# Performance work log

Measured on AMD Instinct MI355X. Metric: run time of the kernel, lower is better.

Reference implementation:

```python
import jax, jax.numpy as jnp
import numpy as np

D, T, HID, Q = 33, 49, 64, 64


def _lin(x, w, b):
    return x @ w.T + b


def setup_inputs() -> dict:
    key = jax.random.key(0)
    ks = jax.random.split(key, 40)

    def nrm(k, shape, scale=0.1):
        return jax.random.normal(k, shape, jnp.float32) * scale

    vals = nrm(ks[0], (D, T), 1.0)
    mask = (jax.random.uniform(ks[1], (D, T)) < 0.8).astype(jnp.float32)
    delta = jax.random.uniform(ks[2], (D, T)) * 2.0
    data = jnp.stack([vals, mask, delta])  # [3, 33, 49]

    return {
        "data": data,
        "h0": nrm(ks[3], (HID,), 1.0),
        "H0": nrm(ks[4], (D, HID), 1.0),
        "gh_w": nrm(ks[5], (HID, D)), "gh_b": nrm(ks[6], (HID,)),
        "gst_w": nrm(ks[7], (HID, D)), "gst_b": nrm(ks[8], (HID,)),
        "gru_wih": nrm(ks[9], (3 * HID, D)), "gru_whh": nrm(ks[10], (3 * HID, HID)),
        "gru_bih": nrm(ks[11], (3 * HID,)), "gru_bhh": nrm(ks[12], (3 * HID,)),
        "wu0_w": nrm(ks[13], (Q, HID)), "wu0_b": nrm(ks[14], (Q,)),
        "wu1_w": nrm(ks[15], (Q, 2 * HID)), "wu1_b": nrm(ks[16], (Q,)),
        "wu_w": nrm(ks[17], (Q, 3 * HID)), "wu_b": nrm(ks[18], (Q,)),
        "wh_w": nrm(ks[19], (D, HID + Q)), "wh_b": nrm(ks[20], (D,)),
        "xst_w": nrm(ks[21], (1, HID)), "xst_b": nrm(ks[22], (1,)),
        "wrg_w": nrm(ks[23], (D, HID)),
        "wrs": nrm(ks[24], (1, HID)),
        "tWz": nrm(ks[25], (D, HID, HID)), "tUzx": nrm(ks[26], (D, HID, 1)), "tUzh": nrm(ks[27], (D, HID, HID)),
        "tWr": nrm(ks[28], (D, HID, HID)), "tUrx": nrm(ks[29], (D, HID, 1)), "tUrh": nrm(ks[30], (D, HID, HID)),
        "tWh": nrm(ks[31], (D, HID, HID)), "tUhx": nrm(ks[32], (D, HID, 1)), "tUhh": nrm(ks[33], (D, HID, HID)),
        "tbz": nrm(ks[34], (HID, 1)), "tbr": nrm(ks[35], (HID, 1)), "tbh": nrm(ks[36], (HID, 1)),
    }


def reference(data, h0, H0, gh_w, gh_b, gst_w, gst_b, gru_wih, gru_whh,
              gru_bih, gru_bhh, wu0_w, wu0_b, wu1_w, wu1_b, wu_w, wu_b,
              wh_w, wh_b, xst_w, xst_b, wrg_w, wrs, tWz, tUzx, tUzh,
              tWr, tUrx, tUrh, tWh, tUhx, tUhh, tbz, tbr, tbh):
    X, M, Dt = data[0], data[1], data[2]  # each (33, 49)
    h = h0          # (HID,) -> becomes (1, HID) after first GRUCell step
    H = H0          # (D, HID)
    outs, Hs, xps = [], [], []
    for t in range(T):
        x, m, d = X[:, t], M[:, t], Dt[:, t]
        # GRU-D style decay gate: exp(-max(0, Linear(delta)))
        gamma_h = jnp.exp(-jax.nn.relu(_lin(d, gh_w, gh_b)))
        h = gamma_h * h
        x_st = _lin(H, xst_w, xst_b).reshape(-1)       # (D,)
        x_st_c = m * x + (1 - m) * x_st                # imputed input
        # torch nn.GRUCell
        xi = x_st_c.reshape(1, D)
        hi = h.reshape(1, HID)
        gi = _lin(xi, gru_wih, gru_bih)
        gh_ = _lin(hi, gru_whh, gru_bhh)
        i_r, i_z, i_n = jnp.split(gi, 3, axis=1)
        h_r, h_z, h_n = jnp.split(gh_, 3, axis=1)
        r = jax.nn.sigmoid(i_r + h_r)
        z = jax.nn.sigmoid(i_z + h_z)
        n = jnp.tanh(i_n + r * h_n)
        h = (1 - z) * n + z * hi                       # (1, HID)
        # original detaches the history used for u_t
        outs.append(jax.lax.stop_gradient(h))
        if t == 0:
            u_t = _lin(h0.reshape(1, -1), wu0_w, wu0_b)
        elif t == 1:
            hd = jnp.concatenate([h0.reshape(1, -1), outs[0]], 0).reshape(1, -1)
            u_t = _lin(hd, wu1_w, wu1_b)
        elif t == 2:
            hd = jnp.concatenate([h0.reshape(1, -1), outs[0], outs[1]], 0).reshape(1, -1)
            u_t = _lin(hd, wu_w, wu_b)
        else:
            hd = jnp.concatenate(outs[t - 3:t], 0).reshape(1, -1)
            u_t = _lin(hd, wu_w, wu_b)
        x_gt_hat = _lin(jnp.concatenate([h, u_t], axis=1), wh_w, wh_b)  # (1, D)
        gamma_st = jnp.exp(-jax.nn.relu(_lin(d, gst_w, gst_b)))
        H = gamma_st * H
        # tMGRU cell: per-variable (D=33) batched matmuls
        Hr = H[:, :, None]              # (D, HID, 1)
        xr = x_st_c[:, None, None]      # (D, 1, 1)
        hr = h.reshape(HID, 1)          # (HID, 1)
        z_t = jax.nn.sigmoid(tWz @ Hr + tUzx @ xr + tUzh @ hr + tbz)
        r_t = jax.nn.sigmoid(tWr @ Hr + tUrx @ xr + tUrh @ hr + tbr)
        Hh = jnp.tanh(r_t * (tWh @ Hr) + tUhx @ xr + tUhh @ hr + tbh)
        H = (z_t * Hr + (1 - z_t) * Hh).reshape(D, HID)
        Hs.append(H)
        a = h @ wrg_w.T                 # (1, D)
        b = wrs @ H.T                   # (1, D)
        alpha1 = jax.nn.softmax(a / (a + b), axis=-1)
        alpha2 = jax.nn.softmax(b / (a + b), axis=-1)
        xps.append(alpha1 * x_gt_hat + alpha2 * x_st)  # (1, D)
    H_s = jnp.stack(Hs)                         # (T, D, HID)
    x_pred = jnp.concatenate(xps, axis=0).T     # (D, T)
    return H_s, x_pred
```

## Files before the change

### kernel.cpp

```cpp
#include <hip/hip_runtime.h>
#include <math.h>

#define DD 33
#define TT 49
#define HH 64
#define NB 33
#define NT 256

#define O_WIHT  0
#define O_WHHT  6336
#define O_GH    18624
#define O_GS    21760
#define O_WT0   24896
#define O_WT1   27008
#define O_WTG   31232
#define O_CU    37568
#define O_R     37700
#define O_GIS   40936
#define O_ZIDX  50344
#define O_ZCNT  52108
#define O_PF    52160
#define PF_STRIDE 160
#define PREP_N  47157

#define SC_AGENT __HIP_MEMORY_SCOPE_AGENT

__device__ __forceinline__ float sigm(float x) {
  return 1.f / (1.f + __expf(-x));
}
__device__ __forceinline__ float ftanh(float x) {
  x = fminf(fmaxf(x, -15.f), 15.f);
  float e = __expf(2.f * x);
  return (e - 1.f) / (e + 1.f);
}

__device__ __forceinline__ float rsum64(float v) {
#pragma unroll
  for (int o = 32; o > 0; o >>= 1) v += __shfl_xor(v, o, 64);
  return v;
}
__device__ __forceinline__ float rmax64(float v) {
#pragma unroll
  for (int o = 32; o > 0; o >>= 1) v = fmaxf(v, __shfl_xor(v, o, 64));
  return v;
}

extern "C" __global__ void gmgru_prep(
    const float* __restrict__ data, const float* __restrict__ gh_w,
    const float* __restrict__ gh_b, const float* __restrict__ gst_w,
    const float* __restrict__ gst_b, const float* __restrict__ wih,
    const float* __restrict__ bih, const float* __restrict__ whh,
    const float* __restrict__ wu0, const float* __restrict__ wu0b,
    const float* __restrict__ wu1, const float* __restrict__ wu1b,
    const float* __restrict__ wu, const float* __restrict__ wub,
    const float* __restrict__ wh_w, float* __restrict__ ws) {
  int idx = blockIdx.x * blockDim.x + threadIdx.x;
  if (idx < 6336) {
    int k = idx / 192, j = idx % 192;
    ws[O_WIHT + idx] = wih[j * DD + k];
  } else if (idx < 18624) {
    int r = idx - 6336, k = r / 192, j = r % 192;
    ws[O_WHHT + r] = whh[j * HH + k];
  } else if (idx < 21760) {
    int r = idx - 18624, t = r / 64, i = r % 64;
    float s = gh_b[i];
    for (int d2 = 0; d2 < DD; ++d2)
      s += data[2 * DD * TT + d2 * TT + t] * gh_w[i * DD + d2];
    ws[O_GH + r] = expf(-fmaxf(s, 0.f));
  } else if (idx < 24896) {
    int r = idx - 21760, t = r / 64, i = r % 64;
    float s = gst_b[i];
    for (int d2 = 0; d2 < DD; ++d2)
      s += data[2 * DD * TT + d2 * TT + t] * gst_w[i * DD + d2];
    ws[O_GS + r] = expf(-fmaxf(s, 0.f));
  } else if (idx < 27008) {
    int r = idx - 24896, dd = r / 64, k = r % 64;
    float s = 0.f;
    for (int q = 0; q < 64; ++q) s += wu0[q * 64 + k] * wh_w[dd * 128 + 64 + q];
    ws[O_WT0 + r] = s;
  } else if (idx < 31232) {
    int r = idx - 27008, dd = r / 128, k = r % 128;
    float s = 0.f;
    for (int q = 0; q < 64; ++q) s += wu1[q * 128 + k] * wh_w[dd * 128 + 64 + q];
    ws[O_WT1 + r] = s;
  } else if (idx < 37568) {
    int r = idx - 31232, dd = r / 192, k = r % 192;
    float s = 0.f;
    for (int q = 0; q < 64; ++q) s += wu[q * 192 + k] * wh_w[dd * 128 + 64 + q];
    ws[O_WTG + r] = s;
  } else if (idx < 37700) {
    int r = idx - 37568, dd = r / 4, v = r % 4;
    float s = 0.f;
    if (v < 3) {
      const float* bp = (v == 0) ? wu0b : (v == 1) ? wu1b : wub;
      for (int q = 0; q < 64; ++q) s += bp[q] * wh_w[dd * 128 + 64 + q];
    }
    ws[O_CU + r] = s;
  } else if (idx < 47108) {
    int r = idx - 37700, t = r / 192, j = r % 192;
    float s = bih[j];
    for (int k = 0; k < DD; ++k) {
      float mv = data[DD * TT + k * TT + t];
      if (mv > 0.5f) s += wih[j * DD + k] * data[k * TT + t];
    }
    ws[O_GIS + r] = s;
  } else if (idx < PREP_N) {
    int t = idx - 47108;
    int c = 0;
    for (int k = 0; k < DD; ++k) {
      float mv = data[DD * TT + k * TT + t];
      if (mv < 0.5f) {
        ws[O_ZIDX + t * 36 + c] = (float)k;
        ++c;
      }
    }
    ws[O_ZCNT + t] = (float)c;
  }
}

extern "C" __global__ void __launch_bounds__(NT, 1)
gmgru_main(const float* __restrict__ data, const float* __restrict__ h0,
           const float* __restrict__ H0, const float* __restrict__ bhh,
           const float* __restrict__ wh_w, const float* __restrict__ wh_b,
           const float* __restrict__ xst_w, const float* __restrict__ xst_b,
           const float* __restrict__ wrg_w, const float* __restrict__ wrs,
           const float* __restrict__ tWz, const float* __restrict__ tUzx,
           const float* __restrict__ tUzh, const float* __restrict__ tWr,
           const float* __restrict__ tUrx, const float* __restrict__ tUrh,
           const float* __restrict__ tWh, const float* __restrict__ tUhx,
           const float* __restrict__ tUhh, const float* __restrict__ tbz,
           const float* __restrict__ tbr, const float* __restrict__ tbh,
           float* __restrict__ ws, unsigned long long* __restrict__ pf,
           float* __restrict__ out) {
  __shared__ float whhT_l[12288];
  __shared__ float wihT_l[6336];
  __shared__ float part[2][6][4][HH];
  __shared__ float ghL[3 * HH];
  __shared__ float hnewL[HH];
  __shared__ float xrow[TT], mrow[TT];
  __shared__ float xcdd[2];
  __shared__ signed char zidxL[TT * 36];
  __shared__ signed char zcntL[TT];

  const int tid = threadIdx.x;
  const int dd = blockIdx.x;
  const int wid = tid >> 6;
  const int lane = tid & 63;

  for (int i = tid; i < 12288; i += NT) whhT_l[i] = ws[O_WHHT + i];
  for (int i = tid; i < 6336; i += NT) wihT_l[i] = ws[O_WIHT + i];
  if (tid < TT) {
    xrow[tid] = data[dd * TT + tid];
    mrow[tid] = data[DD * TT + dd * TT + tid];
    int c = (int)ws[O_ZCNT + tid];
    zcntL[tid] = (signed char)c;
    for (int j = 0; j < c; ++j)
      zidxL[tid * 36 + j] = (signed char)(int)ws[O_ZIDX + tid * 36 + j];
  }
  float4 u0[4], u1[4], u2[4];
  {
    const int base = dd * 4096 + lane * 64 + wid * 16;
#pragma unroll
    for (int g = 0; g < 4; ++g) {
      u0[g] = *reinterpret_cast<const float4*>(tUzh + base + g * 4);
      u1[g] = *reinterpret_cast<const float4*>(tUrh + base + g * 4);
      u2[g] = *reinterpret_cast<const float4*>(tUhh + base + g * 4);
    }
  }
  const float bhh_r = (tid < 192) ? bhh[tid] : 0.f;
  const float ux0 = tUzx[dd * HH + lane];
  const float ux1 = tUrx[dd * HH + lane];
  const float ux2 = tUhx[dd * HH + lane];
  const float tb0 = tbz[lane];
  const float tb1 = tbr[lane];
  const float tb2 = tbh[lane];
  const float xstw_r = xst_w[lane];
  const float wrg_r = wrg_w[dd * HH + lane];
  const float wrs_r = wrs[lane];
  const float whr0_r = wh_w[dd * 128 + lane];
  const float wtg0_r = ws[O_WTG + dd * 192 + lane];
  const float wtg1_r = ws[O_WTG + dd * 192 + 64 + lane];
  const float wtg2_r = ws[O_WTG + dd * 192 + 128 + lane];
  const float wt0_r = ws[O_WT0 + dd * 64 + lane];
  const float wt1a_r = ws[O_WT1 + dd * 128 + lane];
  const float wt1b_r = ws[O_WT1 + dd * 128 + 64 + lane];
  const float cu0_r = ws[O_CU + dd * 4 + 0];
  const float cu1_r = ws[O_CU + dd * 4 + 1];
  const float cu2_r = ws[O_CU + dd * 4 + 2];
  const float whb_r = wh_b[dd];
  const float xstb_r = xst_b[0];
  const float h0s_r = h0[lane];
  float hprev = h0s_r;
  float Hrow = H0[dd * HH + lane];
  float gH_cur = ws[O_GH + lane];
  float gS_cur = ws[O_GS + lane];
  __syncthreads();

  float xst_cur = rsum64(Hrow * xstw_r) + xstb_r;
  if (wid == 0 && lane == 0) {
    float xc0 = mrow[0] * xrow[0] + (1.f - mrow[0]) * xst_cur;
    xcdd[0] = xc0;
    unsigned long long pk0 =
        (1ULL << 32) | (unsigned long long)__float_as_uint(xc0);
    __hip_atomic_store(&pf[(size_t)dd * PF_STRIDE], pk0, __ATOMIC_RELAXED,
                       SC_AGENT);
  }
  float xg_m1 = 0.f, xg_m2 = 0.f, xs_m1 = 0.f, xs_m2 = 0.f;
  float h1 = 0.f, h2 = 0.f, h3 = 0.f;

  for (int t = 0; t < TT; ++t) {
    const int b = t & 1;
    float hpre_r = gH_cur * hprev;
    float Hdec_r = gS_cur * Hrow;
    float gH_nxt = 0.f, gS_nxt = 0.f, xmn = 0.f, omn = 0.f;
    if (t + 1 < TT) {
      gH_nxt = ws[O_GH + (t + 1) * HH + lane];
      gS_nxt = ws[O_GS + (t + 1) * HH + lane];
      float mv = mrow[t + 1];
      xmn = mv * xrow[t + 1];
      omn = 1.f - mv;
    }
    float gis0 = 0.f, gis1 = 0.f, gis2 = 0.f;
    if (wid == 0) {
      gis0 = ws[O_GIS + t * 192 + lane];
      gis1 = ws[O_GIS + t * 192 + 64 + lane];
      gis2 = ws[O_GIS + t * 192 + 128 + lane];
    }

    {
      float pw0 = 0.f, pw1 = 0.f, pw2 = 0.f;
      const int base = dd * 4096 + lane * 64 + wid * 16;
#pragma unroll
      for (int g = 0; g < 4; ++g) {
        float4 a = *reinterpret_cast<const float4*>(tWz + base + g * 4);
        float4 bb = *reinterpret_cast<const float4*>(tWr + base + g * 4);
        float4 c = *reinterpret_cast<const float4*>(tWh + base + g * 4);
        float v0 = __shfl(Hdec_r, wid * 16 + g * 4 + 0, 64);
        float v1 = __shfl(Hdec_r, wid * 16 + g * 4 + 1, 64);
        float v2 = __shfl(Hdec_r, wid * 16 + g * 4 + 2, 64);
        float v3 = __shfl(Hdec_r, wid * 16 + g * 4 + 3, 64);
        pw0 += a.x * v0 + a.y * v1 + a.z * v2 + a.w * v3;
        pw1 += bb.x * v0 + bb.y * v1 + bb.z * v2 + bb.w * v3;
        pw2 += c.x * v0 + c.y * v1 + c.z * v2 + c.w * v3;
      }
      part[b][0][wid][lane] = pw0;
      part[b][1][wid][lane] = pw1;
      part[b][2][wid][lane] = pw2;
    }
    if (tid < 3 * HH) {
      float a0 = 0.f, a1 = 0.f, a2 = 0.f, a3 = 0.f;
#pragma unroll
      for (int k = 0; k < HH; k += 4) {
        a0 += whhT_l[(k + 0) * 192 + tid] * __shfl(hpre_r, k + 0, 64);
        a1 += whhT_l[(k + 1) * 192 + tid] * __shfl(hpre_r, k + 1, 64);
        a2 += whhT_l[(k + 2) * 192 + tid] * __shfl(hpre_r, k + 2, 64);
        a3 += whhT_l[(k + 3) * 192 + tid] * __shfl(hpre_r, k + 3, 64);
      }
      ghL[tid] = bhh_r + ((a0 + a1) + (a2 + a3));
    }
    __syncthreads();

    if (wid == 0) {
      const unsigned tagv = (unsigned)(t + 1);
      const unsigned long long fab = ((unsigned long long)tagv) << 32;
      auto pollLd = [&]() -> unsigned long long {
        return (lane < NB)
                   ? __hip_atomic_load(&pf[(size_t)lane * PF_STRIDE + t],
                                       __ATOMIC_RELAXED, SC_AGENT)
                   : fab;
      };
      unsigned long long pk;
      {
        unsigned long long q0 = pollLd(), q1 = pollLd(), q2 = pollLd(),
                           q3 = pollLd();
        for (;;) {
          if (__all((int)((unsigned)(q0 >> 32) == tagv))) { pk = q0; break; }
          q0 = pollLd();
          if (__all((int)((unsigned)(q1 >> 32) == tagv))) { pk = q1; break; }
          q1 = pollLd();
          if (__all((int)((unsigned)(q2 >> 32) == tagv))) { pk = q2; break; }
          q2 = pollLd();
          if (__all((int)((unsigned)(q3 >> 32) == tagv))) { pk = q3; break; }
          q3 = pollLd();
        }
      }
      float xcv = __uint_as_float((unsigned)(pk & 0xFFFFFFFFull));
      asm volatile("" ::: "memory");
      float gr = gis0, gz = gis1, gn = gis2;
      const int zc = (int)zcntL[t];
#pragma unroll 1
      for (int j = 0; j < zc; ++j) {
        const int k = (int)zidxL[t * 36 + j];
        float xk = __shfl(xcv, k, 64);
        gr += wihT_l[k * 192 + lane] * xk;
        gz += wihT_l[k * 192 + 64 + lane] * xk;
        gn += wihT_l[k * 192 + 128 + lane] * xk;
      }
      float rg = sigm(gr + ghL[lane]);
      float zg = sigm(gz + ghL[64 + lane]);
      float ng = ftanh(gn + rg * ghL[128 + lane]);
      hnewL[lane] = (1.f - zg) * ng + zg * hpre_r;
    }
    __syncthreads();

    const float hn = hnewL[lane];

    {
      float pu0 = 0.f, pu1 = 0.f, pu2 = 0.f;
#pragma unroll
      for (int g = 0; g < 4; ++g) {
        float v0 = hnewL[wid * 16 + g * 4 + 0];
        float v1 = hnewL[wid * 16 + g * 4 + 1];
        float v2 = hnewL[wid * 16 + g * 4 + 2];
        float v3 = hnewL[wid * 16 + g * 4 + 3];
        pu0 += u0[g].x * v0 + u0[g].y * v1 + u0[g].z * v2 + u0[g].w * v3;
        pu1 += u1[g].x * v0 + u1[g].y * v1 + u1[g].z * v2 + u1[g].w * v3;
        pu2 += u2[g].x * v0 + u2[g].y * v1 + u2[g].z * v2 + u2[g].w * v3;
      }
      part[b][3][wid][lane] = pu0;
      part[b][4][wid][lane] = pu1;
      part[b][5][wid][lane] = pu2;
    }
    __syncthreads();

    float r1v = -INFINITY, r2v = -INFINITY;
    if (wid == 1 && t >= 2 && lane < DD) {
      r1v = __hip_atomic_load(&ws[O_R + (t - 2) * 66 + lane], __ATOMIC_RELAXED,
                              SC_AGENT);
      r2v = __hip_atomic_load(&ws[O_R + (t - 2) * 66 + 33 + lane],
                              __ATOMIC_RELAXED, SC_AGENT);
    }

    float sz = part[b][0][0][lane] + part[b][0][1][lane] + part[b][0][2][lane] +
               part[b][0][3][lane] + part[b][3][0][lane] + part[b][3][1][lane] +
               part[b][3][2][lane] + part[b][3][3][lane];
    float sr = part[b][1][0][lane] + part[b][1][1][lane] + part[b][1][2][lane] +
               part[b][1][3][lane] + part[b][4][0][lane] + part[b][4][1][lane] +
               part[b][4][2][lane] + part[b][4][3][lane];
    float swh = part[b][2][0][lane] + part[b][2][1][lane] +
                part[b][2][2][lane] + part[b][2][3][lane];
    float suh = part[b][5][0][lane] + part[b][5][1][lane] +
                part[b][5][2][lane] + part[b][5][3][lane];
    float xc = xcdd[b];
    float z2 = sigm(sz + ux0 * xc + tb0);
    float r2g = sigm(sr + ux1 * xc + tb1);
    float hh = ftanh(r2g * swh + ux2 * xc + suh + tb2);
    float Hn = z2 * Hdec_r + (1.f - z2) * hh;

    if (wid == 0) {
      float xsn = rsum64(xstw_r * Hn);
      if (lane == 0 && t < TT - 1) {
        float xstv = xsn + xstb_r;
        float xcn = xmn + omn * xstv;
        xcdd[(t + 1) & 1] = xcn;
        unsigned long long pkn =
            (((unsigned long long)(unsigned)(t + 2)) << 32) |
            (unsigned long long)__float_as_uint(xcn);
        __hip_atomic_store(&pf[(size_t)dd * PF_STRIDE + (t + 1)], pkn,
                           __ATOMIC_RELAXED, SC_AGENT);
      }
    } else if (wid == 1) {
      if (t >= 2) {
        float m1 = rmax64(r1v), m2 = rmax64(r2v);
        float e1 = (lane < DD) ? __expf(r1v - m1) : 0.f;
        float e2 = (lane < DD) ? __expf(r2v - m2) : 0.f;
        float s1 = rsum64(e1), s2 = rsum64(e2);
        float r1o = __shfl(r1v, dd, 64);
        float r2o = __shfl(r2v, dd, 64);
        if (lane == 0) {
          float a1 = __expf(r1o - m1) / s1;
          float a2 = __expf(r2o - m2) / s2;
          out[TT * DD * HH + dd * TT + (t - 2)] = a1 * xg_m2 + a2 * xs_m2;
        }
      }
      float xg = whr0_r * hn;
      if (t == 0) {
        xg += wt0_r * h0s_r;
      } else if (t == 1) {
        xg += wt1a_r * h0s_r + wt1b_r * h1;
      } else if (t == 2) {
        xg += wtg0_r * h0s_r + wtg1_r * h2 + wtg2_r * h1;
      } else {
        xg += wtg0_r * h3 + wtg1_r * h2 + wtg2_r * h1;
      }
      float xgt = rsum64(xg);
      float cu = (t == 0) ? cu0_r : (t == 1) ? cu1_r : cu2_r;
      float xsn1 = rsum64(xstw_r * Hn);
      xg_m2 = xg_m1;
      xs_m2 = xs_m1;
      xg_m1 = xgt + whb_r + cu;
      xs_m1 = xst_cur;
      xst_cur = xsn1 + xstb_r;
      h3 = h2;
      h2 = h1;
      h1 = hn;
    } else if (wid == 2) {
      float av = rsum64(wrg_r * hn);
      float bvv = rsum64(wrs_r * Hn);
      if (lane == 0) {
        float s = av + bvv;
        __hip_atomic_store(&ws[O_R + t * 66 + dd], av / s, __ATOMIC_RELAXED,
                           SC_AGENT);
        __hip_atomic_store(&ws[O_R + t * 66 + 33 + dd], bvv / s,
                           __ATOMIC_RELAXED, SC_AGENT);
      }
      asm volatile("s_waitcnt vmcnt(0)" ::: "memory");
    } else {
      out[t * DD * HH + dd * HH + lane] = Hn;
    }
    hprev = hn;
    Hrow = Hn;
    gH_cur = gH_nxt;
    gS_cur = gS_nxt;
  }

  __syncthreads();
  if (wid == 0 && lane == 0) {
    __hip_atomic_store(&pf[(size_t)dd * PF_STRIDE + TT],
                       (((unsigned long long)(unsigned)(TT + 1)) << 32),
                       __ATOMIC_RELAXED, SC_AGENT);
  }
  if (wid == 1) {
    const unsigned tagv = (unsigned)(TT + 1);
    for (;;) {
      unsigned long long pk =
          (lane < NB) ? __hip_atomic_load(&pf[(size_t)lane * PF_STRIDE + TT],
                                          __ATOMIC_RELAXED, SC_AGENT)
                      : (((unsigned long long)tagv) << 32);
      if (__all((int)((unsigned)(pk >> 32) == tagv))) break;
      __builtin_amdgcn_s_sleep(1);
    }
    asm volatile("" ::: "memory");
#pragma unroll 1
    for (int e = 0; e < 2; ++e) {
      const int step = TT - 2 + e;
      float r1v = -INFINITY, r2v = -INFINITY;
      if (lane < DD) {
        r1v = __hip_atomic_load(&ws[O_R + step * 66 + lane], __ATOMIC_RELAXED,
                                SC_AGENT);
        r2v = __hip_atomic_load(&ws[O_R + step * 66 + 33 + lane],
                                __ATOMIC_RELAXED, SC_AGENT);
      }
      float m1 = rmax64(r1v), m2 = rmax64(r2v);
      float e1 = (lane < DD) ? __expf(r1v - m1) : 0.f;
      float e2 = (lane < DD) ? __expf(r2v - m2) : 0.f;
      float s1 = rsum64(e1), s2 = rsum64(e2);
      float r1o = __shfl(r1v, dd, 64);
      float r2o = __shfl(r2v, dd, 64);
      if (lane == 0) {
        float a1 = __expf(r1o - m1) / s1;
        float a2 = __expf(r2o - m2) / s2;
        float xgv = (e == 0) ? xg_m2 : xg_m1;
        float xsv = (e == 0) ? xs_m2 : xs_m1;
        out[TT * DD * HH + dd * TT + step] = a1 * xgv + a2 * xsv;
      }
    }
  }
}

extern "C" void kernel_launch(void* const* d_in, const int* in_sizes, int n_in,
                              void* d_out, int out_size, void* d_ws,
                              size_t ws_size, hipStream_t stream) {
  (void)in_sizes; (void)n_in; (void)out_size; (void)ws_size;
  const float* data   = (const float*)d_in[0];
  const float* h0     = (const float*)d_in[1];
  const float* H0     = (const float*)d_in[2];
  const float* gh_w   = (const float*)d_in[3];
  const float* gh_b   = (const float*)d_in[4];
  const float* gst_w  = (const float*)d_in[5];
  const float* gst_b  = (const float*)d_in[6];
  const float* wih    = (const float*)d_in[7];
  const float* whh    = (const float*)d_in[8];
  const float* bih    = (const float*)d_in[9];
  const float* bhh    = (const float*)d_in[10];
  const float* wu0w   = (const float*)d_in[11];
  const float* wu0b   = (const float*)d_in[12];
  const float* wu1w   = (const float*)d_in[13];
  const float* wu1b   = (const float*)d_in[14];
  const float* wuw    = (const float*)d_in[15];
  const float* wub    = (const float*)d_in[16];
  const float* wh_w   = (const float*)d_in[17];
  const float* wh_b   = (const float*)d_in[18];
  const float* xst_w  = (const float*)d_in[19];
  const float* xst_b  = (const float*)d_in[20];
  const float* wrg_w  = (const float*)d_in[21];
  const float* wrs    = (const float*)d_in[22];
  const float* tWz    = (const float*)d_in[23];
  const float* tUzx   = (const float*)d_in[24];
  const float* tUzh   = (const float*)d_in[25];
  const float* tWr    = (const float*)d_in[26];
  const float* tUrx   = (const float*)d_in[27];
  const float* tUrh   = (const float*)d_in[28];
  const float* tWh    = (const float*)d_in[29];
  const float* tUhx   = (const float*)d_in[30];
  const float* tUhh   = (const float*)d_in[31];
  const float* tbz    = (const float*)d_in[32];
  const float* tbr    = (const float*)d_in[33];
  const float* tbh    = (const float*)d_in[34];

  float* ws = (float*)d_ws;
  unsigned long long* pf = (unsigned long long*)(ws + O_PF);

  hipMemsetAsync(pf, 0, (size_t)NB * PF_STRIDE * 8, stream);
  gmgru_prep<<<(PREP_N + 255) / 256, 256, 0, stream>>>(
      data, gh_w, gh_b, gst_w, gst_b, wih, bih, whh, wu0w, wu0b, wu1w, wu1b,
      wuw, wub, wh_w, ws);
  gmgru_main<<<NB, NT, 0, stream>>>(
      data, h0, H0, bhh, wh_w, wh_b, xst_w, xst_b, wrg_w, wrs, tWz, tUzx,
      tUzh, tWr, tUrx, tUrh, tWh, tUhx, tUhh, tbz, tbr, tbh, ws, pf,
      (float*)d_out);
}
```

Baseline: 221.9 us.

## Replicate cross-block poll and GRU update in every wave to drop a barrier

All four waves now poll the global flag array and each computes the small GRU cell update redundantly. The new hidden state is broadcast with wave shuffles instead of going through shared memory. This removes one __syncthreads per timestep and the shared hnewL/xcdd buffers. The own-block x value is taken from the polled packet. In exchange, global polling traffic is four times higher and there is redundant transcendental work. An s_sleep is added to the spin loop, which replaces the previous four-deep pipelined polling and may add wake-up latency.

```diff
diff --git a/kernel.cpp b/kernel.cpp
--- a/kernel.cpp
+++ b/kernel.cpp
@@ -136,9 +136,7 @@
   __shared__ float wihT_l[6336];
   __shared__ float part[2][6][4][HH];
   __shared__ float ghL[3 * HH];
-  __shared__ float hnewL[HH];
   __shared__ float xrow[TT], mrow[TT];
-  __shared__ float xcdd[2];
   __shared__ signed char zidxL[TT * 36];
   __shared__ signed char zcntL[TT];
 
@@ -199,7 +197,6 @@
   float xst_cur = rsum64(Hrow * xstw_r) + xstb_r;
   if (wid == 0 && lane == 0) {
     float xc0 = mrow[0] * xrow[0] + (1.f - mrow[0]) * xst_cur;
-    xcdd[0] = xc0;
     unsigned long long pk0 =
         (1ULL << 32) | (unsigned long long)__float_as_uint(xc0);
     __hip_atomic_store(&pf[(size_t)dd * PF_STRIDE], pk0, __ATOMIC_RELAXED,
@@ -220,12 +217,9 @@
       xmn = mv * xrow[t + 1];
       omn = 1.f - mv;
     }
-    float gis0 = 0.f, gis1 = 0.f, gis2 = 0.f;
-    if (wid == 0) {
-      gis0 = ws[O_GIS + t * 192 + lane];
-      gis1 = ws[O_GIS + t * 192 + 64 + lane];
-      gis2 = ws[O_GIS + t * 192 + 128 + lane];
-    }
+    float gis0 = ws[O_GIS + t * 192 + lane];
+    float gis1 = ws[O_GIS + t * 192 + 64 + lane];
+    float gis2 = ws[O_GIS + t * 192 + 128 + lane];
 
     {
       float pw0 = 0.f, pw1 = 0.f, pw2 = 0.f;
@@ -260,33 +254,21 @@
     }
     __syncthreads();
 
-    if (wid == 0) {
-      const unsigned tagv = (unsigned)(t + 1);
-      const unsigned long long fab = ((unsigned long long)tagv) << 32;
-      auto pollLd = [&]() -> unsigned long long {
-        return (lane < NB)
-                   ? __hip_atomic_load(&pf[(size_t)lane * PF_STRIDE + t],
-                                       __ATOMIC_RELAXED, SC_AGENT)
-                   : fab;
-      };
-      unsigned long long pk;
-      {
-        unsigned long long q0 = pollLd(), q1 = pollLd(), q2 = pollLd(),
-                           q3 = pollLd();
-        for (;;) {
-          if (__all((int)((unsigned)(q0 >> 32) == tagv))) { pk = q0; break; }
-          q0 = pollLd();
-          if (__all((int)((unsigned)(q1 >> 32) == tagv))) { pk = q1; break; }
-          q1 = pollLd();
-          if (__all((int)((unsigned)(q2 >> 32) == tagv))) { pk = q2; break; }
-          q2 = pollLd();
-          if (__all((int)((unsigned)(q3 >> 32) == tagv))) { pk = q3; break; }
-          q3 = pollLd();
-        }
-      }
-      float xcv = __uint_as_float((unsigned)(pk & 0xFFFFFFFFull));
-      asm volatile("" ::: "memory");
-      float gr = gis0, gz = gis1, gn = gis2;
+    const unsigned tagv = (unsigned)(t + 1);
+    unsigned long long pk;
+    for (;;) {
+      pk = (lane < NB)
+               ? __hip_atomic_load(&pf[(size_t)lane * PF_STRIDE + t],
+                                   __ATOMIC_RELAXED, SC_AGENT)
+               : (((unsigned long long)tagv) << 32);
+      if (__all((int)((unsigned)(pk >> 32) == tagv))) break;
+      __builtin_amdgcn_s_sleep(1);
+    }
+    float xcv = __uint_as_float((unsigned)(pk & 0xFFFFFFFFull));
+    asm volatile("" ::: "memory");
+
+    float gr = gis0, gz = gis1, gn = gis2;
+    {
       const int zc = (int)zcntL[t];
 #pragma unroll 1
       for (int j = 0; j < zc; ++j) {
@@ -296,23 +278,20 @@
         gz += wihT_l[k * 192 + 64 + lane] * xk;
         gn += wihT_l[k * 192 + 128 + lane] * xk;
       }
-      float rg = sigm(gr + ghL[lane]);
-      float zg = sigm(gz + ghL[64 + lane]);
-      float ng = ftanh(gn + rg * ghL[128 + lane]);
-      hnewL[lane] = (1.f - zg) * ng + zg * hpre_r;
-    }
-    __syncthreads();
-
-    const float hn = hnewL[lane];
+    }
+    float rg = sigm(gr + ghL[lane]);
+    float zg = sigm(gz + ghL[64 + lane]);
+    float ng = ftanh(gn + rg * ghL[128 + lane]);
+    float hn = (1.f - zg) * ng + zg * hpre_r;
 
     {
       float pu0 = 0.f, pu1 = 0.f, pu2 = 0.f;
 #pragma unroll
       for (int g = 0; g < 4; ++g) {
-        float v0 = hnewL[wid * 16 + g * 4 + 0];
-        float v1 = hnewL[wid * 16 + g * 4 + 1];
-        float v2 = hnewL[wid * 16 + g * 4 + 2];
-        float v3 = hnewL[wid * 16 + g * 4 + 3];
+        float v0 = __shfl(hn, wid * 16 + g * 4 + 0, 64);
+        float v1 = __shfl(hn, wid * 16 + g * 4 + 1, 64);
+        float v2 = __shfl(hn, wid * 16 + g * 4 + 2, 64);
+        float v3 = __shfl(hn, wid * 16 + g * 4 + 3, 64);
         pu0 += u0[g].x * v0 + u0[g].y * v1 + u0[g].z * v2 + u0[g].w * v3;
         pu1 += u1[g].x * v0 + u1[g].y * v1 + u1[g].z * v2 + u1[g].w * v3;
         pu2 += u2[g].x * v0 + u2[g].y * v1 + u2[g].z * v2 + u2[g].w * v3;
@@ -341,7 +320,7 @@
                 part[b][2][2][lane] + part[b][2][3][lane];
     float suh = part[b][5][0][lane] + part[b][5][1][lane] +
                 part[b][5][2][lane] + part[b][5][3][lane];
-    float xc = xcdd[b];
+    float xc = __shfl(xcv, dd, 64);
     float z2 = sigm(sz + ux0 * xc + tb0);
     float r2g = sigm(sr + ux1 * xc + tb1);
     float hh = ftanh(r2g * swh + ux2 * xc + suh + tb2);
@@ -352,7 +331,6 @@
       if (lane == 0 && t < TT - 1) {
         float xstv = xsn + xstb_r;
         float xcn = xmn + omn * xstv;
-        xcdd[(t + 1) & 1] = xcn;
         unsigned long long pkn =
             (((unsigned long long)(unsigned)(t + 2)) << 32) |
             (unsigned long long)__float_as_uint(xcn);
```

After: 225.6 us. No clear change (+1.7%).
